# Kernel tuning notes

Measured on AMD Instinct MI355X. Metric: run time of the kernel, lower is better.

Reference implementation:

```python
import jax, jax.numpy as jnp
import numpy as np

B, S, D = 2, 2048, 2048
H, HKV, DH = 16, 4, 128   # query heads, kv heads, head dim
N_REP = H // HKV
ROPE_BASE = 10000.0


def rotate_half(x):
    x1, x2 = x[..., : DH // 2], x[..., DH // 2 :]
    return jnp.concatenate((-x2, x1), axis=-1)


def rope_tables(seq_len, dtype=jnp.float32):
    inv_freq = 1.0 / (ROPE_BASE ** (jnp.arange(0, DH, 2, dtype=jnp.float32) / DH))
    t = jnp.arange(seq_len, dtype=jnp.float32)
    freqs = jnp.outer(t, inv_freq)                 # [S, DH/2]
    emb = jnp.concatenate((freqs, freqs), axis=-1)  # [S, DH]
    return jnp.cos(emb).astype(dtype), jnp.sin(emb).astype(dtype)


def setup_inputs() -> dict:
    key = jax.random.key(0)
    k1, k2, k3, k4, k5 = jax.random.split(key, 5)
    scale = 1.0 / np.sqrt(D)
    return {
        "hidden_states": jax.random.normal(k1, (B, S, D), dtype=jnp.float32),
        "position_ids": jnp.tile(jnp.arange(S, dtype=jnp.int32)[None, :], (B, 1)),
        "wq": jax.random.normal(k2, (D, H * DH), dtype=jnp.float32) * scale,
        "wk": jax.random.normal(k3, (D, HKV * DH), dtype=jnp.float32) * scale,
        "wv": jax.random.normal(k4, (D, HKV * DH), dtype=jnp.float32) * scale,
        "wo": jax.random.normal(k5, (H * DH, D), dtype=jnp.float32) * scale,
    }


def reference(hidden_states, position_ids, wq, wk, wv, wo):
    x = hidden_states
    b, s, _ = x.shape

    # QKV projections -> [B, H(kv), S, DH]
    q = (x @ wq).reshape(b, s, H, DH).transpose(0, 2, 1, 3)
    k = (x @ wk).reshape(b, s, HKV, DH).transpose(0, 2, 1, 3)
    v = (x @ wv).reshape(b, s, HKV, DH).transpose(0, 2, 1, 3)

    # Rotary position embedding
    cos_t, sin_t = rope_tables(s, x.dtype)
    cos = cos_t[position_ids][:, None, :, :]  # [B,1,S,DH]
    sin = sin_t[position_ids][:, None, :, :]
    q = q * cos + rotate_half(q) * sin
    k = k * cos + rotate_half(k) * sin

    # GQA: repeat KV heads to match query heads
    k = jnp.repeat(k, N_REP, axis=1)  # [B,H,S,DH]
    v = jnp.repeat(v, N_REP, axis=1)

    # Causal SDPA
    scores = jnp.einsum("bhqd,bhkd->bhqk", q, k) / jnp.sqrt(
        jnp.asarray(DH, x.dtype)
    )
    causal = jnp.tril(jnp.ones((s, s), dtype=bool))
    scores = jnp.where(causal[None, None], scores, jnp.asarray(-1e9, x.dtype))
    attn = jax.nn.softmax(scores, axis=-1)
    out = jnp.einsum("bhqk,bhkd->bhqd", attn, v)  # [B,H,S,DH]

    out = out.transpose(0, 2, 1, 3).reshape(b, s, H * DH)
    return out @ wo
```

## Files before the change

kernel.cpp:

```cpp
#include <hip/hip_runtime.h>
#include <cmath>

typedef unsigned short u16;
typedef float floatx4 __attribute__((ext_vector_type(4)));
typedef short short8 __attribute__((ext_vector_type(8)));
typedef short short4v __attribute__((ext_vector_type(4)));
typedef __bf16 bf16x8 __attribute__((ext_vector_type(8)));

#define GLOBAL_AS __attribute__((address_space(1)))
#define LDS_AS __attribute__((address_space(3)))

#define S_LEN 2048
#define D_MODEL 2048
#define NH 16
#define NKV 4
#define DHEAD 128
#define SM_SCALE 0.08838834764831843f
#define K2 (SM_SCALE * 1.4426950408889634f)

__device__ __forceinline__ u16 f2bf(float f) {
    unsigned int u = __builtin_bit_cast(unsigned int, f);
    u += 0x7fffu + ((u >> 16) & 1u);
    return (u16)(u >> 16);
}
__device__ __forceinline__ u16 f2bfr(float f) {
    unsigned int u = __builtin_bit_cast(unsigned int, f);
    return (u16)((u + 0x8000u) >> 16);
}
__device__ __forceinline__ float bf2f(u16 x) {
    unsigned int u = ((unsigned int)x) << 16;
    return __builtin_bit_cast(float, u);
}
__device__ __forceinline__ floatx4 zf4() {
    floatx4 z; z[0] = 0.f; z[1] = 0.f; z[2] = 0.f; z[3] = 0.f; return z;
}
__device__ __forceinline__ floatx4 mfma16(short8 a, short8 b, floatx4 c) {
    return __builtin_amdgcn_mfma_f32_16x16x32_bf16(
        __builtin_bit_cast(bf16x8, a), __builtin_bit_cast(bf16x8, b), c, 0, 0, 0);
}
__device__ __forceinline__ floatx4 mfma16k16(short4v a, short4v b, floatx4 c) {
    return __builtin_amdgcn_mfma_f32_16x16x16bf16_1k(a, b, c, 0, 0, 0);
}
__device__ __forceinline__ void async16(const u16* g, u16* l) {
    __builtin_amdgcn_global_load_lds((GLOBAL_AS void*)g, (LDS_AS void*)l, 16, 0, 0);
}

__global__ void cast_x_kernel(const float4* __restrict__ in, ushort4* __restrict__ out) {
    int i = blockIdx.x * 256 + threadIdx.x;
    float4 v = in[i];
    ushort4 o;
    o.x = f2bf(v.x); o.y = f2bf(v.y); o.z = f2bf(v.z); o.w = f2bf(v.w);
    out[i] = o;
}

__global__ void transpose_cast_kernel(const float* __restrict__ in, u16* __restrict__ out,
                                      int R, int C) {
    __shared__ float tile[32][33];
    int tx = threadIdx.x & 31, ty = threadIdx.x >> 5;
    int bx = blockIdx.x * 32;
    int by = blockIdx.y * 32;
#pragma unroll
    for (int i = 0; i < 32; i += 8)
        tile[ty + i][tx] = in[(size_t)(by + ty + i) * C + bx + tx];
    __syncthreads();
#pragma unroll
    for (int i = 0; i < 32; i += 8)
        out[(size_t)(bx + ty + i) * R + by + tx] = f2bf(tile[tx][ty + i]);
}

__global__ void rope_tables_kernel(float* __restrict__ cs_tab, float* __restrict__ sn_tab) {
    int idx = blockIdx.x * 256 + threadIdx.x;
    int p = idx >> 6, j = idx & 63;
    double e = (double)(2 * j) / 128.0;
    double invf = pow(10000.0, -e);
    float arg = (float)p * (float)invf;
    cs_tab[idx] = (float)cos((double)arg);
    sn_tab[idx] = (float)sin((double)arg);
}

__global__ void rope_apply_kernel(u16* __restrict__ Qb, u16* __restrict__ Kb,
                                  const int* __restrict__ pos,
                                  const float4* __restrict__ cs_tab,
                                  const float4* __restrict__ sn_tab) {
    int idx = blockIdx.x * 256 + threadIdx.x;
    int j4 = idx & 15;
    int s = (idx >> 4) & 2047;
    int r = idx >> 15;
    int hh = r % 20, b = r / 20;
    int p = pos[b * S_LEN + s];
    float4 cs = cs_tab[p * 16 + j4];
    float4 sn = sn_tab[p * 16 + j4];
    u16* base;
    if (hh < 16) base = Qb + (((size_t)(b * NH + hh)) * S_LEN + s) * DHEAD;
    else         base = Kb + (((size_t)(b * NKV + (hh - 16))) * S_LEN + s) * DHEAD;
    base += j4 * 4;
    ushort4 a = *(const ushort4*)(base);
    ushort4 c = *(const ushort4*)(base + 64);
    ushort4 oa, oc;
    float x1, x2;
    x1 = bf2f(a.x); x2 = bf2f(c.x); oa.x = f2bf(x1 * cs.x - x2 * sn.x); oc.x = f2bf(x2 * cs.x + x1 * sn.x);
    x1 = bf2f(a.y); x2 = bf2f(c.y); oa.y = f2bf(x1 * cs.y - x2 * sn.y); oc.y = f2bf(x2 * cs.y + x1 * sn.y);
    x1 = bf2f(a.z); x2 = bf2f(c.z); oa.z = f2bf(x1 * cs.z - x2 * sn.z); oc.z = f2bf(x2 * cs.z + x1 * sn.z);
    x1 = bf2f(a.w); x2 = bf2f(c.w); oa.w = f2bf(x1 * cs.w - x2 * sn.w); oc.w = f2bf(x2 * cs.w + x1 * sn.w);
    *(ushort4*)(base) = oa;
    *(ushort4*)(base + 64) = oc;
}

__device__ __forceinline__ void gemm_mainloop(const u16* __restrict__ A,
                                              const u16* __restrict__ Bt,
                                              int K, u16* ldsA, u16* ldsB,
                                              floatx4 acc[4][4]) {
    const int t = threadIdx.x;
    const int lane = t & 63, wave = t >> 6;
    const int wr = wave >> 1, wc = wave & 1;
    const int lr = lane & 15, q = lane >> 4;
    const int m0 = blockIdx.y * 128, n0 = blockIdx.x * 128;
    const int swz = lr & 7;

#pragma unroll
    for (int r = 0; r < 4; ++r)
#pragma unroll
        for (int c = 0; c < 4; ++c) acc[r][c] = zf4();

    for (int k0 = 0; k0 < K; k0 += 64) {
#pragma unroll
        for (int i = 0; i < 4; ++i) {
            int ci = i * 256 + t;
            int row = ci >> 3;
            int kc = ((ci & 7) ^ (row & 7)) << 3;
            async16(A + (size_t)(m0 + row) * K + k0 + kc, ldsA + (i * 256 + wave * 64) * 8);
            async16(Bt + (size_t)(n0 + row) * K + k0 + kc, ldsB + (i * 256 + wave * 64) * 8);
        }
        __syncthreads();
#pragma unroll
        for (int ks = 0; ks < 2; ++ks) {
            short8 af[4], bfr[4];
#pragma unroll
            for (int r = 0; r < 4; ++r)
                af[r] = *(const short8*)(ldsA + (wr * 64 + r * 16 + lr) * 64 +
                                         (((ks * 4 + q) ^ swz) << 3));
#pragma unroll
            for (int c = 0; c < 4; ++c)
                bfr[c] = *(const short8*)(ldsB + (wc * 64 + c * 16 + lr) * 64 +
                                          (((ks * 4 + q) ^ swz) << 3));
#pragma unroll
            for (int r = 0; r < 4; ++r)
#pragma unroll
                for (int c = 0; c < 4; ++c)
                    acc[r][c] = mfma16(af[r], bfr[c], acc[r][c]);
        }
        __syncthreads();
    }
}

__global__ void qkv_gemm_kernel(const u16* __restrict__ A, const u16* __restrict__ Bt,
                                u16* __restrict__ Qb, u16* __restrict__ Kb,
                                u16* __restrict__ Vt) {
    __shared__ u16 ldsA[128 * 64];
    __shared__ u16 ldsB[128 * 64];
    floatx4 acc[4][4];
    gemm_mainloop(A, Bt, D_MODEL, ldsA, ldsB, acc);

    const int t = threadIdx.x, lane = t & 63, wave = t >> 6;
    const int wr = wave >> 1, wc = wave & 1, lr = lane & 15, q = lane >> 4;
    const int m0 = blockIdx.y * 128 + wr * 64, n0 = blockIdx.x * 128 + wc * 64;
#pragma unroll
    for (int r = 0; r < 4; ++r)
#pragma unroll
        for (int c = 0; c < 4; ++c) {
            int gc = n0 + c * 16 + lr;
#pragma unroll
            for (int rr = 0; rr < 4; ++rr) {
                int grow = m0 + r * 16 + q * 4 + rr;
                int bb = grow >> 11, s = grow & 2047;
                u16 bv = f2bf(acc[r][c][rr]);
                int d = gc & 127;
                if (gc < 2048) {
                    int hh = gc >> 7;
                    Qb[(((size_t)(bb * NH + hh)) * S_LEN + s) * DHEAD + d] = bv;
                } else if (gc < 2560) {
                    int hh = (gc - 2048) >> 7;
                    Kb[(((size_t)(bb * NKV + hh)) * S_LEN + s) * DHEAD + d] = bv;
                } else {
                    int hh = (gc - 2560) >> 7;
                    int s2 = s ^ ((d & 8) >> 1);
                    Vt[(((size_t)(bb * NKV + hh)) * DHEAD + d) * S_LEN + s2] = bv;
                }
            }
        }
}

__global__ void out_gemm_kernel(const u16* __restrict__ A, const u16* __restrict__ Bt,
                                float* __restrict__ out) {
    __shared__ u16 ldsA[128 * 64];
    __shared__ u16 ldsB[128 * 64];
    floatx4 acc[4][4];
    gemm_mainloop(A, Bt, D_MODEL, ldsA, ldsB, acc);

    const int t = threadIdx.x, lane = t & 63, wave = t >> 6;
    const int wr = wave >> 1, wc = wave & 1, lr = lane & 15, q = lane >> 4;
    const int m0 = blockIdx.y * 128 + wr * 64, n0 = blockIdx.x * 128 + wc * 64;
#pragma unroll
    for (int r = 0; r < 4; ++r)
#pragma unroll
        for (int c = 0; c < 4; ++c) {
            int gc = n0 + c * 16 + lr;
#pragma unroll
            for (int rr = 0; rr < 4; ++rr) {
                int grow = m0 + r * 16 + q * 4 + rr;
                out[(size_t)grow * D_MODEL + gc] = acc[r][c][rr];
            }
        }
}

__global__ __launch_bounds__(256, 4) void fa_kernel(const u16* __restrict__ Qb,
                                                    const u16* __restrict__ Kb,
                                                    const u16* __restrict__ Vt,
                                                    u16* __restrict__ Ob) {
    __shared__ u16 ldsK[64 * 128];
    __shared__ u16 ldsV[128 * 64];

    const int t = threadIdx.x, lane = t & 63, wave = t >> 6;
    const int lr = lane & 15, q = lane >> 4;
    const int swz = lr & 7;

    const int bid = blockIdx.x;
    const int r4 = bid >> 8, j = bid & 255;
    const int p = j >> 3, lo = j & 7;
    const int bh = r4 * 8 + lo;
    int qt;
    if (r4 == 0) qt = p;
    else if (r4 == 1) qt = 31 - p;
    else if (r4 == 2) qt = p ^ 16;
    else qt = 31 - (p ^ 16);
    const int b = bh >> 4, h = bh & 15;
    const int kvh = h >> 2;

    const u16* Kp = Kb + (size_t)(b * NKV + kvh) * S_LEN * DHEAD;
    const u16* Vp = Vt + (size_t)(b * NKV + kvh) * DHEAD * S_LEN;
    const u16* Qp = Qb + ((size_t)((b * NH + h) * S_LEN) + qt * 64 + wave * 16) * DHEAD;

    short8 qf[4];
#pragma unroll
    for (int kk = 0; kk < 4; ++kk)
        qf[kk] = *(const short8*)(Qp + (size_t)lr * DHEAD + kk * 32 + q * 8);

    floatx4 accO[8];
#pragma unroll
    for (int d = 0; d < 8; ++d) accO[d] = zf4();
    float m_i = -3e38f, l_i = 0.f;

    const int nkt = qt + 1;
    for (int kt = 0; kt < nkt; ++kt) {
#pragma unroll
        for (int i = 0; i < 4; ++i) {
            int ci = i * 256 + t;
            int krow = ci >> 4, kc = ((ci & 15) ^ ((ci >> 4) & 7)) << 3;
            async16(Kp + (size_t)(kt * 64 + krow) * DHEAD + kc,
                    ldsK + (i * 256 + wave * 64) * 8);
            int dh = ci >> 3, vc = ((ci & 7) ^ ((ci >> 3) & 7)) << 3;
            async16(Vp + (size_t)dh * S_LEN + kt * 64 + vc,
                    ldsV + (i * 256 + wave * 64) * 8);
        }
        __syncthreads();

        floatx4 sc[4];
        __builtin_amdgcn_s_setprio(1);
#pragma unroll
        for (int c = 0; c < 4; ++c) {
            sc[c] = zf4();
#pragma unroll
            for (int kk = 0; kk < 4; ++kk) {
                short8 kfr = *(const short8*)(ldsK + (c * 16 + lr) * DHEAD +
                                              (((kk * 4 + q) ^ swz) << 3));
                sc[c] = mfma16(kfr, qf[kk], sc[c]);
            }
        }
        __builtin_amdgcn_s_setprio(0);

        if (kt == qt) {
            const int qrow = wave * 16 + lr;
#pragma unroll
            for (int c = 0; c < 4; ++c)
#pragma unroll
                for (int rr = 0; rr < 4; ++rr)
                    if (c * 16 + q * 4 + rr > qrow) sc[c][rr] = -3e38f;
        }

        float mx = -3e38f;
#pragma unroll
        for (int c = 0; c < 4; ++c)
#pragma unroll
            for (int rr = 0; rr < 4; ++rr) mx = fmaxf(mx, sc[c][rr]);
        mx = fmaxf(mx, __shfl_xor(mx, 16));
        mx = fmaxf(mx, __shfl_xor(mx, 32));
        float mnew = fmaxf(m_i, mx);
        float mk = mnew * K2;
        bool anyup = __any(mnew > m_i);
        float rs = 0.f;
#pragma unroll
        for (int c = 0; c < 4; ++c)
#pragma unroll
            for (int rr = 0; rr < 4; ++rr) {
                float pe = __builtin_amdgcn_exp2f(fmaf(sc[c][rr], K2, -mk));
                sc[c][rr] = pe;
                rs += pe;
            }
        rs += __shfl_xor(rs, 16);
        rs += __shfl_xor(rs, 32);
        if (anyup) {
            float alpha = __builtin_amdgcn_exp2f(fmaf(m_i, K2, -mk));
            l_i = l_i * alpha + rs;
#pragma unroll
            for (int d = 0; d < 8; ++d) accO[d] *= alpha;
        } else {
            l_i += rs;
        }
        m_i = mnew;

        short4v pb[4];
#pragma unroll
        for (int c = 0; c < 4; ++c) {
            pb[c][0] = (short)f2bfr(sc[c][0]);
            pb[c][1] = (short)f2bfr(sc[c][1]);
            pb[c][2] = (short)f2bfr(sc[c][2]);
            pb[c][3] = (short)f2bfr(sc[c][3]);
        }

        __builtin_amdgcn_s_setprio(1);
#pragma unroll
        for (int ks = 0; ks < 4; ++ks)
#pragma unroll
            for (int d = 0; d < 8; ++d) {
                short4v vf = *(const short4v*)(ldsV + (d * 16 + lr) * 64 +
                                               (((ks * 2 + (q >> 1)) ^ swz) << 3) +
                                               (((q ^ (lr >> 3)) & 1) << 2));
                accO[d] = mfma16k16(vf, pb[ks], accO[d]);
            }
        __builtin_amdgcn_s_setprio(0);
        __syncthreads();
    }

    const int tok = qt * 64 + wave * 16 + lr;
    const float inv = 1.0f / l_i;
    u16* orow = Ob + ((size_t)(b * S_LEN + tok)) * (NH * DHEAD) + h * DHEAD + q * 4;
#pragma unroll
    for (int d = 0; d < 8; ++d) {
        ushort4 o;
        o.x = f2bf(accO[d][0] * inv);
        o.y = f2bf(accO[d][1] * inv);
        o.z = f2bf(accO[d][2] * inv);
        o.w = f2bf(accO[d][3] * inv);
        *(ushort4*)(orow + d * 16) = o;
    }
}

extern "C" void kernel_launch(void* const* d_in, const int* in_sizes, int n_in,
                              void* d_out, int out_size, void* d_ws, size_t ws_size,
                              hipStream_t stream) {
    const float* X  = (const float*)d_in[0];
    const int* pos  = (const int*)d_in[1];
    const float* wq = (const float*)d_in[2];
    const float* wk = (const float*)d_in[3];
    const float* wv = (const float*)d_in[4];
    const float* wo = (const float*)d_in[5];
    float* out = (float*)d_out;

    char* w = (char*)d_ws;
    u16* Xbf    = (u16*)(w);
    u16* Wqkv   = (u16*)(w + 16777216);
    u16* Wo     = (u16*)(w + 29360128);
    u16* Qb     = (u16*)(w + 37748736);
    u16* Kb     = (u16*)(w + 54525952);
    u16* Vt     = (u16*)(w + 58720256);
    u16* Ob     = (u16*)(w + 62914560);
    float* cst  = (float*)(w + 79691776);
    float* snt  = (float*)(w + 80216064);

    cast_x_kernel<<<8192, 256, 0, stream>>>((const float4*)X, (ushort4*)Xbf);
    transpose_cast_kernel<<<dim3(64, 64), 256, 0, stream>>>(wq, Wqkv, 2048, 2048);
    transpose_cast_kernel<<<dim3(16, 64), 256, 0, stream>>>(wk, Wqkv + (size_t)2048 * 2048, 2048, 512);
    transpose_cast_kernel<<<dim3(16, 64), 256, 0, stream>>>(wv, Wqkv + (size_t)2560 * 2048, 2048, 512);
    transpose_cast_kernel<<<dim3(64, 64), 256, 0, stream>>>(wo, Wo, 2048, 2048);
    rope_tables_kernel<<<512, 256, 0, stream>>>(cst, snt);
    qkv_gemm_kernel<<<dim3(24, 32), 256, 0, stream>>>(Xbf, Wqkv, Qb, Kb, Vt);
    rope_apply_kernel<<<5120, 256, 0, stream>>>(Qb, Kb, pos, (const float4*)cst, (const float4*)snt);
    fa_kernel<<<1024, 256, 0, stream>>>(Qb, Kb, Vt, Ob);
    out_gemm_kernel<<<dim3(16, 32), 256, 0, stream>>>(Ob, Wo, out);
}
```

Before: 312.1 us.

## Merge prep kernels, fuse Q RoPE into attention, register-prefetch K/V tiles

Merges the X cast with RoPE table generation and the four weight transposes into a single launch, which cuts launch count. Q rotary embedding moves into the attention kernel's Q fragment load, so the standalone RoPE pass now touches only K. The attention loop drops async global-to-LDS loads and instead prefetches the next K/V tile into registers while computing the current one, then stores it to LDS between barriers. The prefetch adds register pressure and an extra barrier per iteration, and Q is now rounded to bf16 twice.

```diff
diff --git a/kernel.cpp b/kernel.cpp
--- a/kernel.cpp
+++ b/kernel.cpp
@@ -45,19 +45,38 @@
     __builtin_amdgcn_global_load_lds((GLOBAL_AS void*)g, (LDS_AS void*)l, 16, 0, 0);
 }
 
-__global__ void cast_x_kernel(const float4* __restrict__ in, ushort4* __restrict__ out) {
-    int i = blockIdx.x * 256 + threadIdx.x;
-    float4 v = in[i];
-    ushort4 o;
-    o.x = f2bf(v.x); o.y = f2bf(v.y); o.z = f2bf(v.z); o.w = f2bf(v.w);
-    out[i] = o;
-}
-
-__global__ void transpose_cast_kernel(const float* __restrict__ in, u16* __restrict__ out,
-                                      int R, int C) {
+__global__ void cast_tables_kernel(const float4* __restrict__ in, ushort4* __restrict__ out,
+                                   float* __restrict__ cs_tab, float* __restrict__ sn_tab) {
+    int bid = blockIdx.x;
+    if (bid < 8192) {
+        int i = bid * 256 + threadIdx.x;
+        float4 v = in[i];
+        ushort4 o;
+        o.x = f2bf(v.x); o.y = f2bf(v.y); o.z = f2bf(v.z); o.w = f2bf(v.w);
+        out[i] = o;
+    } else {
+        int idx = (bid - 8192) * 256 + threadIdx.x;
+        int p = idx >> 6, jj = idx & 63;
+        double e = (double)(2 * jj) / 128.0;
+        double invf = pow(10000.0, -e);
+        float arg = (float)p * (float)invf;
+        cs_tab[idx] = (float)cos((double)arg);
+        sn_tab[idx] = (float)sin((double)arg);
+    }
+}
+
+__global__ void transpose_all_kernel(const float* __restrict__ wq, const float* __restrict__ wk,
+                                     const float* __restrict__ wv, const float* __restrict__ wo,
+                                     u16* __restrict__ Wqkv, u16* __restrict__ Wo) {
     __shared__ float tile[32][33];
+    int x = blockIdx.x;
+    const float* in; u16* out; int C, bx;
+    if (x < 64)      { in = wq; out = Wqkv;                     C = 2048; bx = x * 32; }
+    else if (x < 80) { in = wk; out = Wqkv + (size_t)2048*2048; C = 512;  bx = (x - 64) * 32; }
+    else if (x < 96) { in = wv; out = Wqkv + (size_t)2560*2048; C = 512;  bx = (x - 80) * 32; }
+    else             { in = wo; out = Wo;                       C = 2048; bx = (x - 96) * 32; }
+    const int R = 2048;
     int tx = threadIdx.x & 31, ty = threadIdx.x >> 5;
-    int bx = blockIdx.x * 32;
     int by = blockIdx.y * 32;
 #pragma unroll
     for (int i = 0; i < 32; i += 8)
@@ -68,32 +87,18 @@
         out[(size_t)(bx + ty + i) * R + by + tx] = f2bf(tile[tx][ty + i]);
 }
 
-__global__ void rope_tables_kernel(float* __restrict__ cs_tab, float* __restrict__ sn_tab) {
-    int idx = blockIdx.x * 256 + threadIdx.x;
-    int p = idx >> 6, j = idx & 63;
-    double e = (double)(2 * j) / 128.0;
-    double invf = pow(10000.0, -e);
-    float arg = (float)p * (float)invf;
-    cs_tab[idx] = (float)cos((double)arg);
-    sn_tab[idx] = (float)sin((double)arg);
-}
-
-__global__ void rope_apply_kernel(u16* __restrict__ Qb, u16* __restrict__ Kb,
-                                  const int* __restrict__ pos,
-                                  const float4* __restrict__ cs_tab,
-                                  const float4* __restrict__ sn_tab) {
+__global__ void rope_k_kernel(u16* __restrict__ Kb, const int* __restrict__ pos,
+                              const float4* __restrict__ cs_tab,
+                              const float4* __restrict__ sn_tab) {
     int idx = blockIdx.x * 256 + threadIdx.x;
     int j4 = idx & 15;
     int s = (idx >> 4) & 2047;
     int r = idx >> 15;
-    int hh = r % 20, b = r / 20;
+    int hh = r & 3, b = r >> 2;
     int p = pos[b * S_LEN + s];
     float4 cs = cs_tab[p * 16 + j4];
     float4 sn = sn_tab[p * 16 + j4];
-    u16* base;
-    if (hh < 16) base = Qb + (((size_t)(b * NH + hh)) * S_LEN + s) * DHEAD;
-    else         base = Kb + (((size_t)(b * NKV + (hh - 16))) * S_LEN + s) * DHEAD;
-    base += j4 * 4;
+    u16* base = Kb + (((size_t)(b * NKV + hh)) * S_LEN + s) * DHEAD + j4 * 4;
     ushort4 a = *(const ushort4*)(base);
     ushort4 c = *(const ushort4*)(base + 64);
     ushort4 oa, oc;
@@ -216,7 +221,10 @@
 __global__ __launch_bounds__(256, 4) void fa_kernel(const u16* __restrict__ Qb,
                                                     const u16* __restrict__ Kb,
                                                     const u16* __restrict__ Vt,
-                                                    u16* __restrict__ Ob) {
+                                                    u16* __restrict__ Ob,
+                                                    const int* __restrict__ pos,
+                                                    const float4* __restrict__ cs_tab,
+                                                    const float4* __restrict__ sn_tab) {
     __shared__ u16 ldsK[64 * 128];
     __shared__ u16 ldsV[128 * 64];
 
@@ -245,24 +253,60 @@
     for (int kk = 0; kk < 4; ++kk)
         qf[kk] = *(const short8*)(Qp + (size_t)lr * DHEAD + kk * 32 + q * 8);
 
+    {
+        const int srow = qt * 64 + wave * 16 + lr;
+        const int pp = pos[b * S_LEN + srow];
+#pragma unroll
+        for (int kk = 0; kk < 2; ++kk)
+#pragma unroll
+            for (int h4 = 0; h4 < 2; ++h4) {
+                float4 cs = cs_tab[pp * 16 + kk * 8 + q * 2 + h4];
+                float4 sn = sn_tab[pp * 16 + kk * 8 + q * 2 + h4];
+#pragma unroll
+                for (int e = 0; e < 4; ++e) {
+                    float cc = (&cs.x)[e], ss = (&sn.x)[e];
+                    int ei = h4 * 4 + e;
+                    float x1 = bf2f((u16)qf[kk][ei]);
+                    float x2 = bf2f((u16)qf[kk + 2][ei]);
+                    qf[kk][ei]     = (short)f2bf(x1 * cc - x2 * ss);
+                    qf[kk + 2][ei] = (short)f2bf(x2 * cc + x1 * ss);
+                }
+            }
+    }
+
+    int4 kreg[4], vreg[4];
+    auto load_tile = [&](int ktile) {
+#pragma unroll
+        for (int i = 0; i < 4; ++i) {
+            int ci = i * 256 + t;
+            int krow = ci >> 4, kc = ((ci & 15) ^ (krow & 7)) << 3;
+            kreg[i] = *(const int4*)(Kp + (size_t)(ktile * 64 + krow) * DHEAD + kc);
+            int dh = ci >> 3, vc = ((ci & 7) ^ (dh & 7)) << 3;
+            vreg[i] = *(const int4*)(Vp + (size_t)dh * S_LEN + ktile * 64 + vc);
+        }
+    };
+    auto store_tile = [&]() {
+#pragma unroll
+        for (int i = 0; i < 4; ++i) {
+            int ci = i * 256 + t;
+            *(int4*)(ldsK + ci * 8) = kreg[i];
+            *(int4*)(ldsV + ci * 8) = vreg[i];
+        }
+    };
+
     floatx4 accO[8];
 #pragma unroll
     for (int d = 0; d < 8; ++d) accO[d] = zf4();
     float m_i = -3e38f, l_i = 0.f;
 
     const int nkt = qt + 1;
+    load_tile(0);
+    store_tile();
+    __syncthreads();
+
     for (int kt = 0; kt < nkt; ++kt) {
-#pragma unroll
-        for (int i = 0; i < 4; ++i) {
-            int ci = i * 256 + t;
-            int krow = ci >> 4, kc = ((ci & 15) ^ ((ci >> 4) & 7)) << 3;
-            async16(Kp + (size_t)(kt * 64 + krow) * DHEAD + kc,
-                    ldsK + (i * 256 + wave * 64) * 8);
-            int dh = ci >> 3, vc = ((ci & 7) ^ ((ci >> 3) & 7)) << 3;
-            async16(Vp + (size_t)dh * S_LEN + kt * 64 + vc,
-                    ldsV + (i * 256 + wave * 64) * 8);
-        }
-        __syncthreads();
+        const bool more = (kt + 1 < nkt);
+        if (more) load_tile(kt + 1);
 
         floatx4 sc[4];
         __builtin_amdgcn_s_setprio(1);
@@ -338,7 +382,12 @@
                 accO[d] = mfma16k16(vf, pb[ks], accO[d]);
             }
         __builtin_amdgcn_s_setprio(0);
-        __syncthreads();
+
+        if (more) {
+            __syncthreads();
+            store_tile();
+            __syncthreads();
+        }
     }
 
     const int tok = qt * 64 + wave * 16 + lr;
@@ -377,14 +426,10 @@
     float* cst  = (float*)(w + 79691776);
     float* snt  = (float*)(w + 80216064);
 
-    cast_x_kernel<<<8192, 256, 0, stream>>>((const float4*)X, (ushort4*)Xbf);
-    transpose_cast_kernel<<<dim3(64, 64), 256, 0, stream>>>(wq, Wqkv, 2048, 2048);
-    transpose_cast_kernel<<<dim3(16, 64), 256, 0, stream>>>(wk, Wqkv + (size_t)2048 * 2048, 2048, 512);
-    transpose_cast_kernel<<<dim3(16, 64), 256, 0, stream>>>(wv, Wqkv + (size_t)2560 * 2048, 2048, 512);
-    transpose_cast_kernel<<<dim3(64, 64), 256, 0, stream>>>(wo, Wo, 2048, 2048);
-    rope_tables_kernel<<<512, 256, 0, stream>>>(cst, snt);
+    cast_tables_kernel<<<8704, 256, 0, stream>>>((const float4*)X, (ushort4*)Xbf, cst, snt);
+    transpose_all_kernel<<<dim3(160, 64), 256, 0, stream>>>(wq, wk, wv, wo, Wqkv, Wo);
     qkv_gemm_kernel<<<dim3(24, 32), 256, 0, stream>>>(Xbf, Wqkv, Qb, Kb, Vt);
-    rope_apply_kernel<<<5120, 256, 0, stream>>>(Qb, Kb, pos, (const float4*)cst, (const float4*)snt);
-    fa_kernel<<<1024, 256, 0, stream>>>(Qb, Kb, Vt, Ob);
+    rope_k_kernel<<<1024, 256, 0, stream>>>(Kb, pos, (const float4*)cst, (const float4*)snt);
+    fa_kernel<<<1024, 256, 0, stream>>>(Qb, Kb, Vt, Ob, pos, (const float4*)cst, (const float4*)snt);
     out_gemm_kernel<<<dim3(16, 32), 256, 0, stream>>>(Ob, Wo, out);
 }
```

Result: slower. 419.2 us (+34.3%).
